# Optimization experiments

Hardware: AMD Instinct MI355X
Metric: run time of the kernel (lower is better)

Reference implementation:

```python
import jax, jax.numpy as jnp
import numpy as np

B, S, D, H, E, K = 4, 2048, 1024, 4096, 8, 2


def setup_inputs() -> dict:
    key = jax.random.key(0)
    ks = jax.random.split(key, 8)
    scale = 0.02
    x = jax.random.normal(ks[0], (B, S, D), dtype=jnp.float32)
    gate_w = jax.random.normal(ks[1], (D, E), dtype=jnp.float32) * scale
    gate_b = jnp.zeros((E,), dtype=jnp.float32)
    w1 = jax.random.normal(ks[2], (E, D, H), dtype=jnp.float32) * scale
    b1 = jnp.zeros((E, H), dtype=jnp.float32)
    w2 = jax.random.normal(ks[3], (E, H, D), dtype=jnp.float32) * scale
    b2 = jnp.zeros((E, D), dtype=jnp.float32)
    return {"x": x, "gate_w": gate_w, "gate_b": gate_b,
            "w1": w1, "b1": b1, "w2": w2, "b2": b2}


def reference(x, gate_w, gate_b, w1, b1, w2, b2):
    b, s, d = x.shape
    xf = x.reshape(-1, d)                              # [T, D]
    T = xf.shape[0]
    gates = xf @ gate_w + gate_b                       # [T, E]
    scores, idx = jax.lax.top_k(gates, K)              # [T, K] each
    g = jax.nn.softmax(scores, axis=-1)                # softmax over top-k slots
    # Per-token, per-expert combine weight (top-k indices are distinct)
    Wte = jnp.zeros((T, E), dtype=xf.dtype).at[jnp.arange(T)[:, None], idx].add(g)
    # Loop over the small fixed expert set via scan, accumulating weighted outputs.
    def body(acc, p):
        w1e, b1e, w2e, b2e, we = p                     # we: [T]
        h = jax.nn.gelu(xf @ w1e + b1e, approximate=False)  # [T, H]
        y = h @ w2e + b2e                              # [T, D]
        return acc + we[:, None] * y, None
    out, _ = jax.lax.scan(body, jnp.zeros_like(xf), (w1, b1, w2, b2, Wte.T))
    return out.reshape(b, s, d)
```

## Files before the change

kernel.cpp:

```cpp
#include <hip/hip_runtime.h>
#include <hip/hip_bf16.h>

#define Bb 4
#define Ss 2048
#define Dd 1024
#define Hh 4096
#define Ee 8
#define Tt (Bb*Ss)

typedef __attribute__((ext_vector_type(8))) short short8;
typedef __attribute__((ext_vector_type(4))) float floatx4;
typedef unsigned short u16;
typedef unsigned int u32;

__device__ __forceinline__ u16 f2bf(float f) {
  union { float f; u32 u; } v; v.f = f;
  return (u16)((v.u + 0x7FFFu + ((v.u >> 16) & 1u)) >> 16);
}

__device__ __forceinline__ void async16(const u16* g, u16* l) {
  __builtin_amdgcn_global_load_lds(
      (const __attribute__((address_space(1))) unsigned int*)g,
      (__attribute__((address_space(3))) unsigned int*)l, 16, 0, 0);
}

__global__ __launch_bounds__(256) void cvt_x(const float* __restrict__ x, u16* __restrict__ xb) {
  size_t i = ((size_t)blockIdx.x * 256 + threadIdx.x) * 8;
  float4 a = *(const float4*)(x + i);
  float4 b = *(const float4*)(x + i + 4);
  union { u16 us[8]; uint4 v; } o;
  o.us[0] = f2bf(a.x); o.us[1] = f2bf(a.y); o.us[2] = f2bf(a.z); o.us[3] = f2bf(a.w);
  o.us[4] = f2bf(b.x); o.us[5] = f2bf(b.y); o.us[6] = f2bf(b.z); o.us[7] = f2bf(b.w);
  *(uint4*)(xb + i) = o.v;
}

__global__ __launch_bounds__(256) void tconv(const float* __restrict__ src, u16* __restrict__ dst,
                                             int R, int C) {
  __shared__ float tile[64][65];
  int e = blockIdx.z;
  int r0 = blockIdx.y * 64, c0 = blockIdx.x * 64;
  int tx = threadIdx.x & 63, ty = threadIdx.x >> 6;
  const float* s = src + (size_t)e * R * C;
  u16* d = dst + (size_t)e * R * C;
#pragma unroll
  for (int i = 0; i < 16; i++) {
    int r = i * 4 + ty;
    tile[r][tx] = s[(size_t)(r0 + r) * C + c0 + tx];
  }
  __syncthreads();
#pragma unroll
  for (int i = 0; i < 16; i++) {
    int c = i * 4 + ty;
    d[(size_t)(c0 + c) * R + r0 + tx] = f2bf(tile[tx][c]);
  }
}

__global__ __launch_bounds__(256) void gate_kernel(const float* __restrict__ x,
                                                   const float* __restrict__ gw,
                                                   const float* __restrict__ gb,
                                                   int* __restrict__ counts,
                                                   int* __restrict__ tokL,
                                                   int* __restrict__ pairL,
                                                   float* __restrict__ wtL) {
  __shared__ float gwl[Dd * Ee];
  for (int i = threadIdx.x; i < Dd * Ee; i += 256) gwl[i] = gw[i];
  __syncthreads();
  int wid = threadIdx.x >> 6, lane = threadIdx.x & 63;
  int t = blockIdx.x * 4 + wid;
  const float* xr = x + (size_t)t * Dd;
  double acc[Ee];
#pragma unroll
  for (int e = 0; e < Ee; e++) acc[e] = 0.0;
  for (int i = 0; i < Dd / 64; i++) {
    int d = lane + i * 64;
    float xv = xr[d];
#pragma unroll
    for (int e = 0; e < Ee; e++) acc[e] += (double)xv * (double)gwl[d * Ee + e];
  }
#pragma unroll
  for (int off = 32; off > 0; off >>= 1)
#pragma unroll
    for (int e = 0; e < Ee; e++) acc[e] += __shfl_down(acc[e], off);
  if (lane == 0) {
    float s[Ee];
#pragma unroll
    for (int e = 0; e < Ee; e++) s[e] = (float)acc[e] + gb[e];
    int i0 = 0;
#pragma unroll
    for (int e = 1; e < Ee; e++) if (s[e] > s[i0]) i0 = e;
    int i1 = (i0 == 0) ? 1 : 0;
#pragma unroll
    for (int e = 0; e < Ee; e++) if (e != i0 && s[e] > s[i1]) i1 = e;
    float ex = expf(s[i1] - s[i0]);
    float g0 = 1.0f / (1.0f + ex);
    float g1 = ex / (1.0f + ex);
    int p0 = atomicAdd(&counts[i0], 1);
    tokL[i0 * Tt + p0] = t; pairL[i0 * Tt + p0] = t * 2;     wtL[i0 * Tt + p0] = g0;
    int p1 = atomicAdd(&counts[i1], 1);
    tokL[i1 * Tt + p1] = t; pairL[i1 * Tt + p1] = t * 2 + 1; wtL[i1 * Tt + p1] = g1;
  }
}

__global__ __launch_bounds__(256) void gemm1(const u16* __restrict__ xb,
                                             const u16* __restrict__ w1t,
                                             const float* __restrict__ b1,
                                             const int* __restrict__ counts,
                                             const int* __restrict__ tokL,
                                             const int* __restrict__ pairL,
                                             u16* __restrict__ h) {
  const int NT = 32;
  int e = blockIdx.z;
  int cnt = counts[e];
  int flat = blockIdx.x + NT * blockIdx.y;
  int x8 = flat & 7, j = flat >> 3;
  int n_t = j % NT;
  int m_t = (j / NT) * 8 + x8;
  int m0 = m_t * 128;
  if (m0 >= cnt) return;
  int rows = cnt - m0; if (rows > 128) rows = 128;
  int n0 = n_t * 128;

  __shared__ __align__(16) u16 As[128 * 32];
  __shared__ __align__(16) u16 Bs[128 * 32];
  __shared__ int ltok[128];
  __shared__ int lpair[128];

  int tid = threadIdx.x;
  if (tid < 128) {
    int ok = tid < rows;
    ltok[tid]  = ok ? tokL[e * Tt + m0 + tid] : tokL[e * Tt + m0];
    lpair[tid] = ok ? pairL[e * Tt + m0 + tid] : 0;
  }
  __syncthreads();

  int wv = tid >> 6, ln = tid & 63;
  int half = wv & 1;
  const u16* gp[4];
  u16* ldst[4];
  if (wv < 2) {
#pragma unroll
    for (int q = 0; q < 4; q++) {
      int r = half * 64 + q * 16 + (ln >> 2);
      int c = (ln & 3) ^ ((r >> 1) & 3);
      gp[q] = xb + (size_t)ltok[r] * Dd + c * 8;
      ldst[q] = As + (half * 64 + q * 16) * 32;
    }
  } else {
#pragma unroll
    for (int q = 0; q < 4; q++) {
      int r = half * 64 + q * 16 + (ln >> 2);
      int c = (ln & 3) ^ ((r >> 1) & 3);
      gp[q] = w1t + ((size_t)e * Hh + n0 + r) * Dd + c * 8;
      ldst[q] = Bs + (half * 64 + q * 16) * 32;
    }
  }

  floatx4 zero4 = {0.f, 0.f, 0.f, 0.f};
  floatx4 acc[4][4];
#pragma unroll
  for (int i = 0; i < 4; i++)
#pragma unroll
    for (int jj = 0; jj < 4; jj++) acc[i][jj] = zero4;

  int wr = wv >> 1, wc = wv & 1;
  int lm = ln & 15, lq = ln >> 4;

  for (int k0 = 0; k0 < Dd; k0 += 32) {
#pragma unroll
    for (int q = 0; q < 4; q++) async16(gp[q], ldst[q]);
#pragma unroll
    for (int q = 0; q < 4; q++) gp[q] += 32;
    __syncthreads();
    short8 a[4], b[4];
#pragma unroll
    for (int i = 0; i < 4; i++) {
      int row = wr * 64 + i * 16 + lm;
      int p = lq ^ ((row >> 1) & 3);
      a[i] = *(const short8*)(As + row * 32 + p * 8);
    }
#pragma unroll
    for (int jj = 0; jj < 4; jj++) {
      int row = wc * 64 + jj * 16 + lm;
      int p = lq ^ ((row >> 1) & 3);
      b[jj] = *(const short8*)(Bs + row * 32 + p * 8);
    }
#pragma unroll
    for (int i = 0; i < 4; i++)
#pragma unroll
      for (int jj = 0; jj < 4; jj++)
        acc[i][jj] = __builtin_amdgcn_mfma_f32_16x16x32_bf16(a[i], b[jj], acc[i][jj], 0, 0, 0);
    __syncthreads();
  }

#pragma unroll
  for (int i = 0; i < 4; i++) {
    int rbase = wr * 64 + i * 16 + lq * 4;
#pragma unroll
    for (int r = 0; r < 4; r++) {
      int row = rbase + r;
      if (row < rows) {
        int p = lpair[row];
#pragma unroll
        for (int jj = 0; jj < 4; jj++) {
          int col = n0 + wc * 64 + jj * 16 + lm;
          float v = acc[i][jj][r] + b1[e * Hh + col];
          v = 0.5f * v * (1.0f + erff(v * 0.70710678118f));
          h[(size_t)p * Hh + col] = f2bf(v);
        }
      }
    }
  }
}

__global__ __launch_bounds__(256) void gemm2(const u16* __restrict__ h,
                                             const u16* __restrict__ w2t,
                                             const float* __restrict__ b2,
                                             const int* __restrict__ counts,
                                             const int* __restrict__ tokL,
                                             const int* __restrict__ pairL,
                                             const float* __restrict__ wtL,
                                             float* __restrict__ out) {
  const int NT = 8;
  int e = blockIdx.z;
  int cnt = counts[e];
  int flat = blockIdx.x + NT * blockIdx.y;
  int x8 = flat & 7, j = flat >> 3;
  int n_t = j % NT;
  int m_t = (j / NT) * 8 + x8;
  int m0 = m_t * 128;
  if (m0 >= cnt) return;
  int rows = cnt - m0; if (rows > 128) rows = 128;
  int n0 = n_t * 128;

  __shared__ __align__(16) u16 As[128 * 32];
  __shared__ __align__(16) u16 Bs[128 * 32];
  __shared__ int ltok[128];
  __shared__ int lpair[128];
  __shared__ float lwt[128];

  int tid = threadIdx.x;
  if (tid < 128) {
    int ok = tid < rows;
    ltok[tid]  = ok ? tokL[e * Tt + m0 + tid] : 0;
    lpair[tid] = ok ? pairL[e * Tt + m0 + tid] : pairL[e * Tt + m0];
    lwt[tid]   = ok ? wtL[e * Tt + m0 + tid] : 0.f;
  }
  __syncthreads();

  int wv = tid >> 6, ln = tid & 63;
  int half = wv & 1;
  const u16* gp[4];
  u16* ldst[4];
  if (wv < 2) {
#pragma unroll
    for (int q = 0; q < 4; q++) {
      int r = half * 64 + q * 16 + (ln >> 2);
      int c = (ln & 3) ^ ((r >> 1) & 3);
      gp[q] = h + (size_t)lpair[r] * Hh + c * 8;
      ldst[q] = As + (half * 64 + q * 16) * 32;
    }
  } else {
#pragma unroll
    for (int q = 0; q < 4; q++) {
      int r = half * 64 + q * 16 + (ln >> 2);
      int c = (ln & 3) ^ ((r >> 1) & 3);
      gp[q] = w2t + ((size_t)e * Dd + n0 + r) * Hh + c * 8;
      ldst[q] = Bs + (half * 64 + q * 16) * 32;
    }
  }

  floatx4 zero4 = {0.f, 0.f, 0.f, 0.f};
  floatx4 acc[4][4];
#pragma unroll
  for (int i = 0; i < 4; i++)
#pragma unroll
    for (int jj = 0; jj < 4; jj++) acc[i][jj] = zero4;

  int wr = wv >> 1, wc = wv & 1;
  int lm = ln & 15, lq = ln >> 4;

  for (int k0 = 0; k0 < Hh; k0 += 32) {
#pragma unroll
    for (int q = 0; q < 4; q++) async16(gp[q], ldst[q]);
#pragma unroll
    for (int q = 0; q < 4; q++) gp[q] += 32;
    __syncthreads();
    short8 a[4], b[4];
#pragma unroll
    for (int i = 0; i < 4; i++) {
      int row = wr * 64 + i * 16 + lm;
      int p = lq ^ ((row >> 1) & 3);
      a[i] = *(const short8*)(As + row * 32 + p * 8);
    }
#pragma unroll
    for (int jj = 0; jj < 4; jj++) {
      int row = wc * 64 + jj * 16 + lm;
      int p = lq ^ ((row >> 1) & 3);
      b[jj] = *(const short8*)(Bs + row * 32 + p * 8);
    }
#pragma unroll
    for (int i = 0; i < 4; i++)
#pragma unroll
      for (int jj = 0; jj < 4; jj++)
        acc[i][jj] = __builtin_amdgcn_mfma_f32_16x16x32_bf16(a[i], b[jj], acc[i][jj], 0, 0, 0);
    __syncthreads();
  }

#pragma unroll
  for (int i = 0; i < 4; i++) {
    int rbase = wr * 64 + i * 16 + lq * 4;
#pragma unroll
    for (int r = 0; r < 4; r++) {
      int row = rbase + r;
      if (row < rows) {
        int t = ltok[row];
        float w = lwt[row];
#pragma unroll
        for (int jj = 0; jj < 4; jj++) {
          int col = n0 + wc * 64 + jj * 16 + lm;
          float v = (acc[i][jj][r] + b2[e * Dd + col]) * w;
          atomicAdd(out + (size_t)t * Dd + col, v);
        }
      }
    }
  }
}

extern "C" void kernel_launch(void* const* d_in, const int* in_sizes, int n_in,
                              void* d_out, int out_size, void* d_ws, size_t ws_size,
                              hipStream_t stream) {
  const float* x      = (const float*)d_in[0];
  const float* gate_w = (const float*)d_in[1];
  const float* gate_b = (const float*)d_in[2];
  const float* w1     = (const float*)d_in[3];
  const float* b1     = (const float*)d_in[4];
  const float* w2     = (const float*)d_in[5];
  const float* b2     = (const float*)d_in[6];
  float* out = (float*)d_out;

  char* ws = (char*)d_ws;
  size_t off = 0;
  int* counts = (int*)(ws + off); off += 256;
  int* tokL   = (int*)(ws + off); off += (size_t)Ee * Tt * 4;
  int* pairL  = (int*)(ws + off); off += (size_t)Ee * Tt * 4;
  float* wtL  = (float*)(ws + off); off += (size_t)Ee * Tt * 4;
  u16* xb     = (u16*)(ws + off); off += (size_t)Tt * Dd * 2;
  u16* w1t    = (u16*)(ws + off); off += (size_t)Ee * Hh * Dd * 2;
  u16* w2t    = (u16*)(ws + off); off += (size_t)Ee * Dd * Hh * 2;
  u16* hbuf   = (u16*)(ws + off); off += (size_t)Tt * 2 * Hh * 2;

  hipMemsetAsync(counts, 0, 256, stream);
  hipMemsetAsync(out, 0, (size_t)Tt * Dd * 4, stream);

  cvt_x<<<(Tt * Dd) / (256 * 8), 256, 0, stream>>>(x, xb);
  tconv<<<dim3(Hh / 64, Dd / 64, Ee), 256, 0, stream>>>(w1, w1t, Dd, Hh);
  tconv<<<dim3(Dd / 64, Hh / 64, Ee), 256, 0, stream>>>(w2, w2t, Hh, Dd);
  gate_kernel<<<Tt / 4, 256, 0, stream>>>(x, gate_w, gate_b, counts, tokL, pairL, wtL);
  gemm1<<<dim3(32, 64, Ee), 256, 0, stream>>>(xb, w1t, b1, counts, tokL, pairL, hbuf);
  gemm2<<<dim3(8, 64, Ee), 256, 0, stream>>>(hbuf, w2t, b2, counts, tokL, pairL, wtL, out);
}
```

Measured before the change: 1.120 ms.

## Double-buffer LDS tiles in both expert GEMMs to overlap loads with MFMA

Both expert GEMM kernels now allocate two LDS stages for the A and B tiles. Each iteration issues the async global-to-LDS loads for the next K-slice before computing the current one, waiting with vmcnt(4) so only the older loads must have landed. The goal is to hide global load latency behind the MFMA work that was previously serialized behind __syncthreads. The cost is twice the LDS per block, which may lower occupancy, plus reliance on hand-written waitcnt counts that must match the number of loads each wave issues.

```diff
diff --git a/kernel.cpp b/kernel.cpp
--- a/kernel.cpp
+++ b/kernel.cpp
@@ -120,8 +120,8 @@
   int rows = cnt - m0; if (rows > 128) rows = 128;
   int n0 = n_t * 128;
 
-  __shared__ __align__(16) u16 As[128 * 32];
-  __shared__ __align__(16) u16 Bs[128 * 32];
+  __shared__ __align__(16) u16 As[2 * 128 * 32];
+  __shared__ __align__(16) u16 Bs[2 * 128 * 32];
   __shared__ int ltok[128];
   __shared__ int lpair[128];
 
@@ -165,31 +165,47 @@
   int wr = wv >> 1, wc = wv & 1;
   int lm = ln & 15, lq = ln >> 4;
 
-  for (int k0 = 0; k0 < Dd; k0 += 32) {
-#pragma unroll
-    for (int q = 0; q < 4; q++) async16(gp[q], ldst[q]);
-#pragma unroll
-    for (int q = 0; q < 4; q++) gp[q] += 32;
-    __syncthreads();
+  const int NK = Dd / 32;
+#pragma unroll
+  for (int q = 0; q < 4; q++) async16(gp[q], ldst[q]);
+#pragma unroll
+  for (int q = 0; q < 4; q++) gp[q] += 32;
+
+  for (int it = 0; it < NK; ++it) {
+    if (it + 1 < NK) {
+      int nb = (it + 1) & 1;
+#pragma unroll
+      for (int q = 0; q < 4; q++) async16(gp[q], ldst[q] + nb * 4096);
+#pragma unroll
+      for (int q = 0; q < 4; q++) gp[q] += 32;
+      asm volatile("s_waitcnt vmcnt(4)" ::: "memory");
+    } else {
+      asm volatile("s_waitcnt vmcnt(0)" ::: "memory");
+    }
+    __builtin_amdgcn_s_barrier();
+    int cb = it & 1;
+    const u16* Ab = As + cb * 4096;
+    const u16* Bp = Bs + cb * 4096;
     short8 a[4], b[4];
 #pragma unroll
     for (int i = 0; i < 4; i++) {
       int row = wr * 64 + i * 16 + lm;
       int p = lq ^ ((row >> 1) & 3);
-      a[i] = *(const short8*)(As + row * 32 + p * 8);
+      a[i] = *(const short8*)(Ab + row * 32 + p * 8);
     }
 #pragma unroll
     for (int jj = 0; jj < 4; jj++) {
       int row = wc * 64 + jj * 16 + lm;
       int p = lq ^ ((row >> 1) & 3);
-      b[jj] = *(const short8*)(Bs + row * 32 + p * 8);
+      b[jj] = *(const short8*)(Bp + row * 32 + p * 8);
     }
 #pragma unroll
     for (int i = 0; i < 4; i++)
 #pragma unroll
       for (int jj = 0; jj < 4; jj++)
         acc[i][jj] = __builtin_amdgcn_mfma_f32_16x16x32_bf16(a[i], b[jj], acc[i][jj], 0, 0, 0);
-    __syncthreads();
+    asm volatile("s_waitcnt lgkmcnt(0)" ::: "memory");
+    __builtin_amdgcn_s_barrier();
   }
 
 #pragma unroll
@@ -232,8 +248,8 @@
   int rows = cnt - m0; if (rows > 128) rows = 128;
   int n0 = n_t * 128;
 
-  __shared__ __align__(16) u16 As[128 * 32];
-  __shared__ __align__(16) u16 Bs[128 * 32];
+  __shared__ __align__(16) u16 As[2 * 128 * 32];
+  __shared__ __align__(16) u16 Bs[2 * 128 * 32];
   __shared__ int ltok[128];
   __shared__ int lpair[128];
   __shared__ float lwt[128];
@@ -279,31 +295,47 @@
   int wr = wv >> 1, wc = wv & 1;
   int lm = ln & 15, lq = ln >> 4;
 
-  for (int k0 = 0; k0 < Hh; k0 += 32) {
-#pragma unroll
-    for (int q = 0; q < 4; q++) async16(gp[q], ldst[q]);
-#pragma unroll
-    for (int q = 0; q < 4; q++) gp[q] += 32;
-    __syncthreads();
+  const int NK = Hh / 32;
+#pragma unroll
+  for (int q = 0; q < 4; q++) async16(gp[q], ldst[q]);
+#pragma unroll
+  for (int q = 0; q < 4; q++) gp[q] += 32;
+
+  for (int it = 0; it < NK; ++it) {
+    if (it + 1 < NK) {
+      int nb = (it + 1) & 1;
+#pragma unroll
+      for (int q = 0; q < 4; q++) async16(gp[q], ldst[q] + nb * 4096);
+#pragma unroll
+      for (int q = 0; q < 4; q++) gp[q] += 32;
+      asm volatile("s_waitcnt vmcnt(4)" ::: "memory");
+    } else {
+      asm volatile("s_waitcnt vmcnt(0)" ::: "memory");
+    }
+    __builtin_amdgcn_s_barrier();
+    int cb = it & 1;
+    const u16* Ab = As + cb * 4096;
+    const u16* Bp = Bs + cb * 4096;
     short8 a[4], b[4];
 #pragma unroll
     for (int i = 0; i < 4; i++) {
       int row = wr * 64 + i * 16 + lm;
       int p = lq ^ ((row >> 1) & 3);
-      a[i] = *(const short8*)(As + row * 32 + p * 8);
+      a[i] = *(const short8*)(Ab + row * 32 + p * 8);
     }
 #pragma unroll
     for (int jj = 0; jj < 4; jj++) {
       int row = wc * 64 + jj * 16 + lm;
       int p = lq ^ ((row >> 1) & 3);
-      b[jj] = *(const short8*)(Bs + row * 32 + p * 8);
+      b[jj] = *(const short8*)(Bp + row * 32 + p * 8);
     }
 #pragma unroll
     for (int i = 0; i < 4; i++)
 #pragma unroll
       for (int jj = 0; jj < 4; jj++)
         acc[i][jj] = __builtin_amdgcn_mfma_f32_16x16x32_bf16(a[i], b[jj], acc[i][jj], 0, 0, 0);
-    __syncthreads();
+    asm volatile("s_waitcnt lgkmcnt(0)" ::: "memory");
+    __builtin_amdgcn_s_barrier();
   }
 
 #pragma unroll
```

Result: no change. 1.110 ms (-0.9%).
